# Performance work log

Measured on AMD Instinct MI355X. Metric: run time of the kernel, lower is better.

Reference implementation:

```python
import jax, jax.numpy as jnp
import numpy as np

N_NODES = 100000
N_EDGES = 1000000
D_FEAT = 64          # per-node embedding dim
IN_FEATS = 2 * D_FEAT  # concat(src, dst)
HID = 128


def setup_inputs() -> dict:
    key = jax.random.key(0)
    ks = jax.random.split(key, 12)
    zi = jax.random.normal(ks[0], (N_NODES, D_FEAT), dtype=jnp.float32)
    zj = jax.random.normal(ks[1], (N_NODES, D_FEAT), dtype=jnp.float32)
    zn = jax.random.normal(ks[2], (N_NODES, D_FEAT), dtype=jnp.float32)
    pos_src = jax.random.randint(ks[3], (N_EDGES,), 0, N_NODES)
    pos_dst = jax.random.randint(ks[4], (N_EDGES,), 0, N_NODES)
    neg_src = jax.random.randint(ks[5], (N_EDGES,), 0, N_NODES)
    neg_dst = jax.random.randint(ks[6], (N_EDGES,), 0, N_NODES)
    # MLP params (nn.Linear style: y = x @ W.T + b)
    s1 = 1.0 / np.sqrt(IN_FEATS)
    s3 = 1.0 / np.sqrt(HID)
    W1 = jax.random.uniform(ks[7], (HID, IN_FEATS), jnp.float32, -s1, s1)
    b1 = jax.random.uniform(ks[8], (HID,), jnp.float32, -s1, s1)
    W3 = jax.random.uniform(ks[9], (1, HID), jnp.float32, -s3, s3)
    b3 = jax.random.uniform(ks[10], (1,), jnp.float32, -s3, s3)
    return {"zi": zi, "zj": zj, "zn": zn, "W1": W1, "b1": b1, "W3": W3,
            "b3": b3, "pos_src": pos_src, "pos_dst": pos_dst,
            "neg_src": neg_src, "neg_dst": neg_dst}


def _lp(raw, W1, b1, W3, b3):
    # Link_Prediction with n_layers=2, dropout=0: linear-relu-linear-sigmoid
    hid = jax.nn.relu(raw @ W1.T + b1)      # [E, HID]
    return jax.nn.sigmoid(hid @ W3.T + b3)  # [E, 1]


def reference(zi, zj, zn, W1, b1, W3, b3, pos_src, pos_dst, neg_src, neg_dst):
    # pos graph: gather src/dst node embeddings per edge, concat -> MLP
    raw_pos = jnp.concatenate([zi[pos_src], zj[pos_dst]], axis=1)  # [E, 2*D]
    pos_score = _lp(raw_pos, W1, b1, W3, b3)
    # NOTE: source bug — neg score is computed from the POS raw features
    # (pos_graph.edata['raw']); the neg gather/concat is dead code, so we
    # faithfully score raw_pos again.
    neg_score = _lp(raw_pos, W1, b1, W3, b3)
    return pos_score, neg_score
```

## Files before the change

kernel.cpp:

```cpp
#include <hip/hip_runtime.h>

typedef float    f32x16 __attribute__((ext_vector_type(16)));
typedef _Float16 f16x8  __attribute__((ext_vector_type(8)));

#define NWAVES 4
#define TPW 8
#define TILES_PER_BLOCK (NWAVES * TPW)

__global__ __launch_bounds__(256) void prep_f16(
    const float* __restrict__ zi, const float* __restrict__ zj,
    _Float16* __restrict__ zif, _Float16* __restrict__ zjf, const int nChunkPer)
{
    const int stride = gridDim.x * blockDim.x;
    for (int c = blockIdx.x * blockDim.x + threadIdx.x; c < 2 * nChunkPer; c += stride) {
        const float* s;
        _Float16* d;
        if (c < nChunkPer) { s = zi + (size_t)c * 8; d = zif + (size_t)c * 8; }
        else { s = zj + (size_t)(c - nChunkPer) * 8; d = zjf + (size_t)(c - nChunkPer) * 8; }
        const float4 a0 = *reinterpret_cast<const float4*>(s);
        const float4 a1 = *reinterpret_cast<const float4*>(s + 4);
        f16x8 v;
        v[0]=(_Float16)a0.x; v[1]=(_Float16)a0.y; v[2]=(_Float16)a0.z; v[3]=(_Float16)a0.w;
        v[4]=(_Float16)a1.x; v[5]=(_Float16)a1.y; v[6]=(_Float16)a1.z; v[7]=(_Float16)a1.w;
        *reinterpret_cast<f16x8*>(d) = v;
    }
}

template<bool F16TAB>
__device__ inline void load_afrag(f16x8 (&a)[8],
    const float* __restrict__ zi, const float* __restrict__ zj,
    const _Float16* __restrict__ zif, const _Float16* __restrict__ zjf,
    const int si, const int di, const int lq)
{
    if constexpr (F16TAB) {
        const _Float16* __restrict__ sp = zif + (size_t)si * 64;
        const _Float16* __restrict__ dp = zjf + (size_t)di * 64;
        #pragma unroll
        for (int kk = 0; kk < 4; ++kk) {
            a[kk]     = *reinterpret_cast<const f16x8*>(sp + kk * 16 + lq * 8);
            a[kk + 4] = *reinterpret_cast<const f16x8*>(dp + kk * 16 + lq * 8);
        }
    } else {
        const float* __restrict__ sp = zi + (size_t)si * 64;
        const float* __restrict__ dp = zj + (size_t)di * 64;
        #pragma unroll
        for (int kk = 0; kk < 8; ++kk) {
            const int kb = kk * 16 + lq * 8;
            const float* p = (kk < 4) ? (sp + kb) : (dp + kb - 64);
            const float4 a0 = *reinterpret_cast<const float4*>(p);
            const float4 a1 = *reinterpret_cast<const float4*>(p + 4);
            f16x8 v;
            v[0]=(_Float16)a0.x; v[1]=(_Float16)a0.y; v[2]=(_Float16)a0.z; v[3]=(_Float16)a0.w;
            v[4]=(_Float16)a1.x; v[5]=(_Float16)a1.y; v[6]=(_Float16)a1.z; v[7]=(_Float16)a1.w;
            a[kk] = v;
        }
    }
}

template<bool F16TAB>
__global__ __launch_bounds__(256) void graphlp_mfma(
    const float* __restrict__ zi, const float* __restrict__ zj,
    const _Float16* __restrict__ zif, const _Float16* __restrict__ zjf,
    const float* __restrict__ W1, const float* __restrict__ b1p,
    const float* __restrict__ W3, const float* __restrict__ b3p,
    const int* __restrict__ psrc, const int* __restrict__ pdst,
    float* __restrict__ out, const int nEdges, const int nTiles)
{
    __shared__ uint4 w1s[2048];
    char* lds = reinterpret_cast<char*>(w1s);
    const int tid = threadIdx.x;

    #pragma unroll
    for (int i = 0; i < 8; ++i) {
        const int ch  = tid + i * 256;
        const int row = ch >> 4;
        const int kg  = ch & 15;
        const float* s = W1 + row * 128 + kg * 8;
        const float4 a0 = *reinterpret_cast<const float4*>(s);
        const float4 a1 = *reinterpret_cast<const float4*>(s + 4);
        f16x8 v;
        v[0]=(_Float16)a0.x; v[1]=(_Float16)a0.y; v[2]=(_Float16)a0.z; v[3]=(_Float16)a0.w;
        v[4]=(_Float16)a1.x; v[5]=(_Float16)a1.y; v[6]=(_Float16)a1.z; v[7]=(_Float16)a1.w;
        const int off = row * 256 + ((kg * 16) ^ ((row & 7) << 4));
        *reinterpret_cast<f16x8*>(lds + off) = v;
    }
    __syncthreads();

    const int lane = tid & 63;
    const int wav  = tid >> 6;
    const int lr   = lane & 31;
    const int lq   = lane >> 5;

    float b1v[4], w3v[4];
    #pragma unroll
    for (int nb = 0; nb < 4; ++nb) {
        b1v[nb] = b1p[nb * 32 + lr];
        w3v[nb] = W3[nb * 32 + lr];
    }
    const float b3 = b3p[0];

    const int gbase = blockIdx.x * TILES_PER_BLOCK + wav;

    f16x8 af[8];
    int si1 = 0, di1 = 0;
    {
        int si0 = 0, di0 = 0;
        if (gbase < nTiles) {
            const int e = min(gbase * 32 + lr, nEdges - 1);
            si0 = psrc[e]; di0 = pdst[e];
        }
        const int gB = gbase + NWAVES;
        if (gB < nTiles) {
            const int e = min(gB * 32 + lr, nEdges - 1);
            si1 = psrc[e]; di1 = pdst[e];
        }
        if (gbase < nTiles)
            load_afrag<F16TAB>(af, zi, zj, zif, zjf, si0, di0, lq);
    }

    #pragma unroll
    for (int t = 0; t < TPW; ++t) {
        const int g = gbase + t * NWAVES;
        if (g >= nTiles) break;

        int si2 = 0, di2 = 0;
        if (t + 2 < TPW) {
            const int g2 = g + 2 * NWAVES;
            if (g2 < nTiles) {
                const int e2 = min(g2 * 32 + lr, nEdges - 1);
                si2 = psrc[e2]; di2 = pdst[e2];
            }
        }

        f16x8 an[8];
        const bool havnext = (t + 1 < TPW) && (g + NWAVES < nTiles);
        if (havnext)
            load_afrag<F16TAB>(an, zi, zj, zif, zjf, si1, di1, lq);

        float pr[16];
        #pragma unroll
        for (int r = 0; r < 16; ++r) pr[r] = 0.0f;

        #pragma unroll
        for (int nbp = 0; nbp < 2; ++nbp) {
            const float bb0 = b1v[2*nbp], bb1 = b1v[2*nbp + 1];
            f32x16 acc0, acc1;
            #pragma unroll
            for (int r = 0; r < 16; ++r) { acc0[r] = bb0; acc1[r] = bb1; }
            const int n0 = (2*nbp)     * 32 + lr;
            const int n1 = (2*nbp + 1) * 32 + lr;
            __builtin_amdgcn_s_setprio(1);
            #pragma unroll
            for (int kk = 0; kk < 8; ++kk) {
                const int kx = kk * 32 + lq * 16;
                const f16x8 bf0 = *reinterpret_cast<const f16x8*>(
                    lds + n0 * 256 + (kx ^ ((n0 & 7) << 4)));
                const f16x8 bf1 = *reinterpret_cast<const f16x8*>(
                    lds + n1 * 256 + (kx ^ ((n1 & 7) << 4)));
                acc0 = __builtin_amdgcn_mfma_f32_32x32x16_f16(af[kk], bf0, acc0, 0, 0, 0);
                acc1 = __builtin_amdgcn_mfma_f32_32x32x16_f16(af[kk], bf1, acc1, 0, 0, 0);
            }
            __builtin_amdgcn_s_setprio(0);
            const float ww0 = w3v[2*nbp], ww1 = w3v[2*nbp + 1];
            #pragma unroll
            for (int r = 0; r < 16; ++r) {
                pr[r] = fmaf(fmaxf(acc0[r], 0.0f), ww0, pr[r]);
                pr[r] = fmaf(fmaxf(acc1[r], 0.0f), ww1, pr[r]);
            }
        }

        float p8[8];
        #pragma unroll
        for (int r = 0; r < 8; ++r) {
            const float lo = pr[r], hi = pr[r + 8];
            const float sent = (lane & 1) ? lo : hi;
            const float got  = __shfl_xor(sent, 1);
            p8[r] = ((lane & 1) ? hi : lo) + got;
        }
        float p4[4];
        #pragma unroll
        for (int r = 0; r < 4; ++r) {
            const float lo = p8[r], hi = p8[r + 4];
            const float sent = (lane & 2) ? lo : hi;
            const float got  = __shfl_xor(sent, 2);
            p4[r] = ((lane & 2) ? hi : lo) + got;
        }
        float p2[2];
        #pragma unroll
        for (int r = 0; r < 2; ++r) {
            const float lo = p4[r], hi = p4[r + 2];
            const float sent = (lane & 4) ? lo : hi;
            const float got  = __shfl_xor(sent, 4);
            p2[r] = ((lane & 4) ? hi : lo) + got;
        }
        float p1;
        {
            const float lo = p2[0], hi = p2[1];
            const float sent = (lane & 8) ? lo : hi;
            const float got  = __shfl_xor(sent, 8);
            p1 = ((lane & 8) ? hi : lo) + got;
        }
        p1 += __shfl_xor(p1, 16);

        const int rid = 8 * (lane & 1) + 4 * ((lane >> 1) & 1)
                      + 2 * ((lane >> 2) & 1) + ((lane >> 3) & 1);
        const int m  = (rid & 3) + 8 * (rid >> 2) + 4 * lq;
        const int eo = g * 32 + m;
        if (eo < nEdges) {
            const float sc = 1.0f / (1.0f + __expf(-(p1 + b3)));
            if (lane & 16) out[nEdges + eo] = sc;
            else           out[eo] = sc;
        }

        #pragma unroll
        for (int kk = 0; kk < 8; ++kk) af[kk] = an[kk];
        si1 = si2; di1 = di2;
    }
}

extern "C" void kernel_launch(void* const* d_in, const int* in_sizes, int n_in,
                              void* d_out, int out_size, void* d_ws, size_t ws_size,
                              hipStream_t stream)
{
    const float* zi = (const float*)d_in[0];
    const float* zj = (const float*)d_in[1];
    const float* W1 = (const float*)d_in[3];
    const float* b1 = (const float*)d_in[4];
    const float* W3 = (const float*)d_in[5];
    const float* b3 = (const float*)d_in[6];
    const int* psrc = (const int*)d_in[7];
    const int* pdst = (const int*)d_in[8];
    float* out = (float*)d_out;

    const int nEdges = in_sizes[7];
    const int nNodesI = in_sizes[0] / 64;
    const int nNodesJ = in_sizes[1] / 64;
    const int nTiles = (nEdges + 31) / 32;
    const int nBlocks = (nTiles + TILES_PER_BLOCK - 1) / TILES_PER_BLOCK;

    const size_t bytesI = (size_t)nNodesI * 64 * sizeof(_Float16);
    const size_t bytesJ = (size_t)nNodesJ * 64 * sizeof(_Float16);
    const bool useF16 = (ws_size >= bytesI + bytesJ) && (nNodesI == nNodesJ);

    if (useF16) {
        _Float16* zif = (_Float16*)d_ws;
        _Float16* zjf = (_Float16*)((char*)d_ws + bytesI);
        const int nChunkPer = nNodesI * 64 / 8;
        hipLaunchKernelGGL(prep_f16, dim3(2048), dim3(256), 0, stream,
                           zi, zj, zif, zjf, nChunkPer);
        hipLaunchKernelGGL((graphlp_mfma<true>), dim3(nBlocks), dim3(256), 0, stream,
                           zi, zj, zif, zjf, W1, b1, W3, b3, psrc, pdst,
                           out, nEdges, nTiles);
    } else {
        hipLaunchKernelGGL((graphlp_mfma<false>), dim3(nBlocks), dim3(256), 0, stream,
                           zi, zj, (const _Float16*)nullptr, (const _Float16*)nullptr,
                           W1, b1, W3, b3, psrc, pdst, out, nEdges, nTiles);
    }
}
```

Measured before the change: 70.90 us.

## Gather node embeddings from FP8 tables instead of FP16 and decode in-register

The prep kernel now quantizes zi/zj to FP8 e4m3 instead of FP16, halving the table footprint and the random gather traffic per edge. The main kernel loads packed FP8 bytes, prefetches one tile ahead, and decodes to FP16 in registers before the MFMA. Tiles per wave drop from 8 to 4 and launch bounds now request 4 blocks per CU to raise occupancy. FP8 quantization of the inputs adds substantial numerical error, which may break accuracy tolerance, and the decode adds ALU work per tile.

New measurement: 178.9 us. 2.52x slower.

```diff
diff --git a/kernel.cpp b/kernel.cpp
--- a/kernel.cpp
+++ b/kernel.cpp
@@ -1,66 +1,81 @@
 #include <hip/hip_runtime.h>
+#include <hip/hip_fp8.h>
 
 typedef float    f32x16 __attribute__((ext_vector_type(16)));
 typedef _Float16 f16x8  __attribute__((ext_vector_type(8)));
 
 #define NWAVES 4
-#define TPW 8
+#define TPW 4
 #define TILES_PER_BLOCK (NWAVES * TPW)
 
-__global__ __launch_bounds__(256) void prep_f16(
+__device__ __forceinline__ uint32_t enc4_fp8(float a, float b, float c, float d) {
+#if __has_builtin(__builtin_amdgcn_cvt_pk_fp8_f32)
+    int w = __builtin_amdgcn_cvt_pk_fp8_f32(a, b, 0, false);
+    w     = __builtin_amdgcn_cvt_pk_fp8_f32(c, d, w, true);
+    return (uint32_t)w;
+#else
+    __hip_fp8_e4m3 e0(a), e1(b), e2(c), e3(d);
+    return (uint32_t)e0.__x | ((uint32_t)e1.__x << 8) |
+           ((uint32_t)e2.__x << 16) | ((uint32_t)e3.__x << 24);
+#endif
+}
+
+__device__ __forceinline__ f16x8 dec8_fp8(uint2 u) {
+    f16x8 v;
+#if __has_builtin(__builtin_amdgcn_cvt_f32_fp8)
+    {
+        const float f0 = __builtin_amdgcn_cvt_f32_fp8((int)u.x, 0);
+        const float f1 = __builtin_amdgcn_cvt_f32_fp8((int)u.x, 1);
+        const float f2 = __builtin_amdgcn_cvt_f32_fp8((int)u.x, 2);
+        const float f3 = __builtin_amdgcn_cvt_f32_fp8((int)u.x, 3);
+        const auto h01 = __builtin_amdgcn_cvt_pkrtz(f0, f1);
+        const auto h23 = __builtin_amdgcn_cvt_pkrtz(f2, f3);
+        v[0] = h01[0]; v[1] = h01[1]; v[2] = h23[0]; v[3] = h23[1];
+    }
+    {
+        const float f0 = __builtin_amdgcn_cvt_f32_fp8((int)u.y, 0);
+        const float f1 = __builtin_amdgcn_cvt_f32_fp8((int)u.y, 1);
+        const float f2 = __builtin_amdgcn_cvt_f32_fp8((int)u.y, 2);
+        const float f3 = __builtin_amdgcn_cvt_f32_fp8((int)u.y, 3);
+        const auto h01 = __builtin_amdgcn_cvt_pkrtz(f0, f1);
+        const auto h23 = __builtin_amdgcn_cvt_pkrtz(f2, f3);
+        v[4] = h01[0]; v[5] = h01[1]; v[6] = h23[0]; v[7] = h23[1];
+    }
+#else
+    union { uint2 w; unsigned char b[8]; } cc; cc.w = u;
+    #pragma unroll
+    for (int j = 0; j < 8; ++j) {
+        __hip_fp8_e4m3 t; t.__x = cc.b[j];
+        v[j] = (_Float16)(float)t;
+    }
+#endif
+    return v;
+}
+
+__global__ __launch_bounds__(256) void prep_fp8(
     const float* __restrict__ zi, const float* __restrict__ zj,
-    _Float16* __restrict__ zif, _Float16* __restrict__ zjf, const int nChunkPer)
+    uint2* __restrict__ zif8, uint2* __restrict__ zjf8, const int nChunkPer)
 {
     const int stride = gridDim.x * blockDim.x;
     for (int c = blockIdx.x * blockDim.x + threadIdx.x; c < 2 * nChunkPer; c += stride) {
         const float* s;
-        _Float16* d;
-        if (c < nChunkPer) { s = zi + (size_t)c * 8; d = zif + (size_t)c * 8; }
-        else { s = zj + (size_t)(c - nChunkPer) * 8; d = zjf + (size_t)(c - nChunkPer) * 8; }
+        uint2* d;
+        int cc;
+        if (c < nChunkPer) { cc = c; s = zi + (size_t)cc * 8; d = zif8 + cc; }
+        else { cc = c - nChunkPer; s = zj + (size_t)cc * 8; d = zjf8 + cc; }
         const float4 a0 = *reinterpret_cast<const float4*>(s);
         const float4 a1 = *reinterpret_cast<const float4*>(s + 4);
-        f16x8 v;
-        v[0]=(_Float16)a0.x; v[1]=(_Float16)a0.y; v[2]=(_Float16)a0.z; v[3]=(_Float16)a0.w;
-        v[4]=(_Float16)a1.x; v[5]=(_Float16)a1.y; v[6]=(_Float16)a1.z; v[7]=(_Float16)a1.w;
-        *reinterpret_cast<f16x8*>(d) = v;
-    }
-}
-
-template<bool F16TAB>
-__device__ inline void load_afrag(f16x8 (&a)[8],
+        uint2 w;
+        w.x = enc4_fp8(a0.x, a0.y, a0.z, a0.w);
+        w.y = enc4_fp8(a1.x, a1.y, a1.z, a1.w);
+        *d = w;
+    }
+}
+
+template<bool FP8>
+__global__ __launch_bounds__(256, 4) void graphlp_mfma(
     const float* __restrict__ zi, const float* __restrict__ zj,
-    const _Float16* __restrict__ zif, const _Float16* __restrict__ zjf,
-    const int si, const int di, const int lq)
-{
-    if constexpr (F16TAB) {
-        const _Float16* __restrict__ sp = zif + (size_t)si * 64;
-        const _Float16* __restrict__ dp = zjf + (size_t)di * 64;
-        #pragma unroll
-        for (int kk = 0; kk < 4; ++kk) {
-            a[kk]     = *reinterpret_cast<const f16x8*>(sp + kk * 16 + lq * 8);
-            a[kk + 4] = *reinterpret_cast<const f16x8*>(dp + kk * 16 + lq * 8);
-        }
-    } else {
-        const float* __restrict__ sp = zi + (size_t)si * 64;
-        const float* __restrict__ dp = zj + (size_t)di * 64;
-        #pragma unroll
-        for (int kk = 0; kk < 8; ++kk) {
-            const int kb = kk * 16 + lq * 8;
-            const float* p = (kk < 4) ? (sp + kb) : (dp + kb - 64);
-            const float4 a0 = *reinterpret_cast<const float4*>(p);
-            const float4 a1 = *reinterpret_cast<const float4*>(p + 4);
-            f16x8 v;
-            v[0]=(_Float16)a0.x; v[1]=(_Float16)a0.y; v[2]=(_Float16)a0.z; v[3]=(_Float16)a0.w;
-            v[4]=(_Float16)a1.x; v[5]=(_Float16)a1.y; v[6]=(_Float16)a1.z; v[7]=(_Float16)a1.w;
-            a[kk] = v;
-        }
-    }
-}
-
-template<bool F16TAB>
-__global__ __launch_bounds__(256) void graphlp_mfma(
-    const float* __restrict__ zi, const float* __restrict__ zj,
-    const _Float16* __restrict__ zif, const _Float16* __restrict__ zjf,
+    const unsigned char* __restrict__ zif8, const unsigned char* __restrict__ zjf8,
     const float* __restrict__ W1, const float* __restrict__ b1p,
     const float* __restrict__ W3, const float* __restrict__ b3p,
     const int* __restrict__ psrc, const int* __restrict__ pdst,
@@ -101,9 +116,11 @@
 
     const int gbase = blockIdx.x * TILES_PER_BLOCK + wav;
 
-    f16x8 af[8];
+    uint2 px[8];
     int si1 = 0, di1 = 0;
-    {
+    #pragma unroll
+    for (int kk = 0; kk < 8; ++kk) { px[kk].x = 0u; px[kk].y = 0u; }
+    if constexpr (FP8) {
         int si0 = 0, di0 = 0;
         if (gbase < nTiles) {
             const int e = min(gbase * 32 + lr, nEdges - 1);
@@ -114,8 +131,20 @@
             const int e = min(gB * 32 + lr, nEdges - 1);
             si1 = psrc[e]; di1 = pdst[e];
         }
-        if (gbase < nTiles)
-            load_afrag<F16TAB>(af, zi, zj, zif, zjf, si0, di0, lq);
+        if (gbase < nTiles) {
+            const unsigned char* sp = zif8 + (size_t)si0 * 64;
+            const unsigned char* dp = zjf8 + (size_t)di0 * 64;
+            #pragma unroll
+            for (int kk = 0; kk < 4; ++kk) {
+                px[kk]     = *reinterpret_cast<const uint2*>(sp + kk * 16 + lq * 8);
+                px[kk + 4] = *reinterpret_cast<const uint2*>(dp + kk * 16 + lq * 8);
+            }
+        }
+    } else {
+        if (gbase < nTiles) {
+            const int e = min(gbase * 32 + lr, nEdges - 1);
+            si1 = psrc[e]; di1 = pdst[e];
+        }
     }
 
     #pragma unroll
@@ -123,19 +152,54 @@
         const int g = gbase + t * NWAVES;
         if (g >= nTiles) break;
 
+        f16x8 afrag[8];
+        uint2 pn[8];
         int si2 = 0, di2 = 0;
-        if (t + 2 < TPW) {
-            const int g2 = g + 2 * NWAVES;
-            if (g2 < nTiles) {
-                const int e2 = min(g2 * 32 + lr, nEdges - 1);
-                si2 = psrc[e2]; di2 = pdst[e2];
-            }
-        }
-
-        f16x8 an[8];
-        const bool havnext = (t + 1 < TPW) && (g + NWAVES < nTiles);
-        if (havnext)
-            load_afrag<F16TAB>(an, zi, zj, zif, zjf, si1, di1, lq);
+
+        if constexpr (FP8) {
+            const bool havnext = (t + 1 < TPW) && (g + NWAVES < nTiles);
+            #pragma unroll
+            for (int kk = 0; kk < 8; ++kk) { pn[kk].x = 0u; pn[kk].y = 0u; }
+            if (havnext) {
+                const unsigned char* sp = zif8 + (size_t)si1 * 64;
+                const unsigned char* dp = zjf8 + (size_t)di1 * 64;
+                #pragma unroll
+                for (int kk = 0; kk < 4; ++kk) {
+                    pn[kk]     = *reinterpret_cast<const uint2*>(sp + kk * 16 + lq * 8);
+                    pn[kk + 4] = *reinterpret_cast<const uint2*>(dp + kk * 16 + lq * 8);
+                }
+            }
+            if (t + 2 < TPW) {
+                const int g2 = g + 2 * NWAVES;
+                if (g2 < nTiles) {
+                    const int e2 = min(g2 * 32 + lr, nEdges - 1);
+                    si2 = psrc[e2]; di2 = pdst[e2];
+                }
+            }
+            #pragma unroll
+            for (int kk = 0; kk < 8; ++kk) afrag[kk] = dec8_fp8(px[kk]);
+        } else {
+            const float* sp = zi + (size_t)si1 * 64;
+            const float* dp = zj + (size_t)di1 * 64;
+            #pragma unroll
+            for (int kk = 0; kk < 8; ++kk) {
+                const int kb = kk * 16 + lq * 8;
+                const float* p = (kk < 4) ? (sp + kb) : (dp + kb - 64);
+                const float4 a0 = *reinterpret_cast<const float4*>(p);
+                const float4 a1 = *reinterpret_cast<const float4*>(p + 4);
+                f16x8 v;
+                v[0]=(_Float16)a0.x; v[1]=(_Float16)a0.y; v[2]=(_Float16)a0.z; v[3]=(_Float16)a0.w;
+                v[4]=(_Float16)a1.x; v[5]=(_Float16)a1.y; v[6]=(_Float16)a1.z; v[7]=(_Float16)a1.w;
+                afrag[kk] = v;
+            }
+            if (t + 1 < TPW) {
+                const int gn = g + NWAVES;
+                if (gn < nTiles) {
+                    const int en = min(gn * 32 + lr, nEdges - 1);
+                    si2 = psrc[en]; di2 = pdst[en];
+                }
+            }
+        }
 
         float pr[16];
         #pragma unroll
@@ -157,8 +221,8 @@
                     lds + n0 * 256 + (kx ^ ((n0 & 7) << 4)));
                 const f16x8 bf1 = *reinterpret_cast<const f16x8*>(
                     lds + n1 * 256 + (kx ^ ((n1 & 7) << 4)));
-                acc0 = __builtin_amdgcn_mfma_f32_32x32x16_f16(af[kk], bf0, acc0, 0, 0, 0);
-                acc1 = __builtin_amdgcn_mfma_f32_32x32x16_f16(af[kk], bf1, acc1, 0, 0, 0);
+                acc0 = __builtin_amdgcn_mfma_f32_32x32x16_f16(afrag[kk], bf0, acc0, 0, 0, 0);
+                acc1 = __builtin_amdgcn_mfma_f32_32x32x16_f16(afrag[kk], bf1, acc1, 0, 0, 0);
             }
             __builtin_amdgcn_s_setprio(0);
             const float ww0 = w3v[2*nbp], ww1 = w3v[2*nbp + 1];
@@ -212,8 +276,10 @@
             else           out[eo] = sc;
         }
 
-        #pragma unroll
-        for (int kk = 0; kk < 8; ++kk) af[kk] = an[kk];
+        if constexpr (FP8) {
+            #pragma unroll
+            for (int kk = 0; kk < 8; ++kk) px[kk] = pn[kk];
+        }
         si1 = si2; di1 = di2;
     }
 }
@@ -238,22 +304,22 @@
     const int nTiles = (nEdges + 31) / 32;
     const int nBlocks = (nTiles + TILES_PER_BLOCK - 1) / TILES_PER_BLOCK;
 
-    const size_t bytesI = (size_t)nNodesI * 64 * sizeof(_Float16);
-    const size_t bytesJ = (size_t)nNodesJ * 64 * sizeof(_Float16);
-    const bool useF16 = (ws_size >= bytesI + bytesJ) && (nNodesI == nNodesJ);
-
-    if (useF16) {
-        _Float16* zif = (_Float16*)d_ws;
-        _Float16* zjf = (_Float16*)((char*)d_ws + bytesI);
+    const size_t bytesI = (size_t)nNodesI * 64;
+    const size_t bytesJ = (size_t)nNodesJ * 64;
+    const bool useF8 = (ws_size >= bytesI + bytesJ);
+
+    if (useF8) {
+        unsigned char* zif8 = (unsigned char*)d_ws;
+        unsigned char* zjf8 = (unsigned char*)d_ws + bytesI;
         const int nChunkPer = nNodesI * 64 / 8;
-        hipLaunchKernelGGL(prep_f16, dim3(2048), dim3(256), 0, stream,
-                           zi, zj, zif, zjf, nChunkPer);
+        hipLaunchKernelGGL(prep_fp8, dim3(2048), dim3(256), 0, stream,
+                           zi, zj, (uint2*)zif8, (uint2*)zjf8, nChunkPer);
         hipLaunchKernelGGL((graphlp_mfma<true>), dim3(nBlocks), dim3(256), 0, stream,
-                           zi, zj, zif, zjf, W1, b1, W3, b3, psrc, pdst,
+                           zi, zj, zif8, zjf8, W1, b1, W3, b3, psrc, pdst,
                            out, nEdges, nTiles);
     } else {
         hipLaunchKernelGGL((graphlp_mfma<false>), dim3(nBlocks), dim3(256), 0, stream,
-                           zi, zj, (const _Float16*)nullptr, (const _Float16*)nullptr,
+                           zi, zj, (const unsigned char*)nullptr, (const unsigned char*)nullptr,
                            W1, b1, W3, b3, psrc, pdst, out, nEdges, nTiles);
     }
 }
```
